# Optimization experiments

Hardware: AMD Instinct MI355X
Metric: run time of the kernel (lower is better)

The kernel has to match this reference:

```python
import jax, jax.numpy as jnp
import numpy as np

N_QUBITS = 16
DIM = 1 << N_QUBITS
NUM_CLASSES = 23
BATCH = 64

# PauliZ sign table: wire 0 is the most-significant bit of the flattened index.
_idx = np.arange(DIM)
SIGNS = np.stack([1 - 2 * ((_idx >> (N_QUBITS - 1 - w)) & 1) for w in range(N_QUBITS)], axis=1).astype(np.float32)  # (DIM, 16)


def _rx_mat(theta):
    c = jnp.cos(theta / 2).astype(jnp.complex64)
    s = (-1j * jnp.sin(theta / 2)).astype(jnp.complex64)
    return jnp.stack([jnp.stack([c, s]), jnp.stack([s, c])])  # (2,2)


def _rot_mat(phi, theta, omega):
    ct = jnp.cos(theta / 2)
    st = jnp.sin(theta / 2)
    a = jnp.exp(-0.5j * (phi + omega)) * ct
    b = -jnp.exp(0.5j * (phi - omega)) * st
    c = jnp.exp(-0.5j * (phi - omega)) * st
    d = jnp.exp(0.5j * (phi + omega)) * ct
    return jnp.stack([jnp.stack([a, b]), jnp.stack([c, d])]).astype(jnp.complex64)


def _apply_1q(state, U, w):
    # state: (B, 2,...,2); shared 2x2 gate on wire w (axis w+1)
    st = jnp.tensordot(state, U, axes=[[w + 1], [1]])  # contracted axis moves to last
    return jnp.moveaxis(st, -1, w + 1)


def _apply_rx_batched(state, theta_b, w):
    # per-sample RX angles theta_b: (B,)
    half = theta_b / 2
    c = jnp.cos(half).astype(jnp.complex64)
    s = (-1j * jnp.sin(half)).astype(jnp.complex64)
    U = jnp.stack([jnp.stack([c, s], -1), jnp.stack([s, c], -1)], -2)  # (B,2,2)
    st = jnp.moveaxis(state, w + 1, -1)
    st = jnp.einsum('bji,b...i->b...j', U, st)
    return jnp.moveaxis(st, -1, w + 1)


def _apply_crx(state, theta, ctrl, tgt):
    s0 = jax.lax.index_in_dim(state, 0, axis=ctrl + 1, keepdims=False)
    s1 = jax.lax.index_in_dim(state, 1, axis=ctrl + 1, keepdims=False)
    tax = tgt + 1 if tgt < ctrl else tgt  # target axis after control axis removal
    U = _rx_mat(theta)
    s1 = jnp.moveaxis(jnp.tensordot(s1, U, axes=[[tax], [1]]), -1, tax)
    return jnp.stack([s0, s1], axis=ctrl + 1)


def _circuit(x, w0, x0, w1, x1):
    B = x.shape[0]
    state = jnp.zeros((B,) + (2,) * N_QUBITS, jnp.complex64)
    state = state.at[(slice(None),) + (0,) * N_QUBITS].set(1.0)
    for w, xc in ((w0, x0), (w1, x1)):
        for q in range(N_QUBITS):
            state = _apply_rx_batched(state, x[:, q], q)
        for q in range(N_QUBITS):
            state = _apply_1q(state, _rot_mat(w[q, 0], w[q, 1], w[q, 2]), q)
        for q in range(N_QUBITS):
            state = _apply_crx(state, xc[q], q, (q + 1) % N_QUBITS)
    probs = (state.real ** 2 + state.imag ** 2).reshape(B, DIM)
    return probs @ jnp.asarray(SIGNS)  # (B, 16) PauliZ expvals


def setup_inputs() -> dict:
    key = jax.random.key(0)
    ks = jax.random.split(key, 7)
    return {
        'x': jax.random.normal(ks[0], (BATCH, N_QUBITS), jnp.float32),
        'w0': jax.random.normal(ks[1], (N_QUBITS, 3), jnp.float32),
        'x0': jax.random.normal(ks[2], (N_QUBITS,), jnp.float32),
        'w1': jax.random.normal(ks[3], (N_QUBITS, 3), jnp.float32),
        'x1': jax.random.normal(ks[4], (N_QUBITS,), jnp.float32),
        'fc_w': jax.random.normal(ks[5], (NUM_CLASSES, N_QUBITS), jnp.float32) * 0.25,
        'fc_b': jax.random.normal(ks[6], (NUM_CLASSES,), jnp.float32) * 0.05,
    }


def reference(x, w0, x0, w1, x1, fc_w, fc_b):
    feats = _circuit(x, w0, x0, w1, x1)           # (B, 16)
    logits = feats @ fc_w.T + fc_b                # (B, 23)
    return jax.nn.log_softmax(logits, axis=1)
```

## Files before the change

### kernel.cpp

```cpp
#include <hip/hip_runtime.h>
#include <hip/hip_bf16.h>


#define NQ 16
#define DIM 65536
#define BATCH 64
#define PSTR 544


template<int RB>
__device__ __forceinline__ void g1q_reg(float* sr, float* si, const float* U) {
  float u00r=U[0],u00i=U[1],u01r=U[2],u01i=U[3],u10r=U[4],u10i=U[5],u11r=U[6],u11i=U[7];
#pragma unroll
  for (int k = 0; k < 8; ++k) {
    int lo = k & ((1<<RB)-1);
    int j0 = ((k >> RB) << (RB+1)) | lo;
    int j1 = j0 | (1<<RB);
    float a0r=sr[j0], a0i=si[j0], a1r=sr[j1], a1i=si[j1];
    sr[j0] = u00r*a0r - u00i*a0i + u01r*a1r - u01i*a1i;
    si[j0] = u00r*a0i + u00i*a0r + u01r*a1i + u01i*a1r;
    sr[j1] = u10r*a0r - u10i*a0i + u11r*a1r - u11i*a1i;
    si[j1] = u10r*a0i + u10i*a0r + u11r*a1i + u11i*a1r;
  }
}

template<int RB, int CB>
__device__ __forceinline__ void gsel_reg_cc(float* sr, float* si, const float* M0, const float* M1) {
  float a0=M0[0],a1=M0[1],a2=M0[2],a3=M0[3],a4=M0[4],a5=M0[5],a6=M0[6],a7=M0[7];
  float b0=M1[0],b1=M1[1],b2=M1[2],b3=M1[3],b4=M1[4],b5=M1[5],b6=M1[6],b7=M1[7];
#pragma unroll
  for (int k = 0; k < 8; ++k) {
    int lo = k & ((1<<RB)-1);
    int j0 = ((k >> RB) << (RB+1)) | lo;
    int j1 = j0 | (1<<RB);
    const bool c = ((j0 >> CB) & 1) != 0;
    float u00r=c?b0:a0, u00i=c?b1:a1, u01r=c?b2:a2, u01i=c?b3:a3;
    float u10r=c?b4:a4, u10i=c?b5:a5, u11r=c?b6:a6, u11i=c?b7:a7;
    float p0r=sr[j0], p0i=si[j0], p1r=sr[j1], p1i=si[j1];
    sr[j0] = u00r*p0r - u00i*p0i + u01r*p1r - u01i*p1i;
    si[j0] = u00r*p0i + u00i*p0r + u01r*p1i + u01i*p1r;
    sr[j1] = u10r*p0r - u10i*p0i + u11r*p1r - u11i*p1i;
    si[j1] = u10r*p0i + u10i*p0r + u11r*p1i + u11i*p1r;
  }
}

template<int RB>
__device__ __forceinline__ void gsel_reg_pred(float* sr, float* si, const float* M0,
                                              const float* M1, bool ctrl) {
  float u[8];
#pragma unroll
  for (int e = 0; e < 8; ++e) u[e] = ctrl ? M1[e] : M0[e];
  g1q_reg<RB>(sr, si, u);
}

template<int LB, int CB>
__device__ __forceinline__ void gsel_lane_creg(float* sr, float* si, const float* M0,
                                               const float* M1, int lane) {
  int side = (lane >> LB) & 1;
  float d0r = side ? M0[6] : M0[0], d0i = side ? M0[7] : M0[1];
  float o0r = side ? M0[4] : M0[2], o0i = side ? M0[5] : M0[3];
  float d1r = side ? M1[6] : M1[0], d1i = side ? M1[7] : M1[1];
  float o1r = side ? M1[4] : M1[2], o1i = side ? M1[5] : M1[3];
#pragma unroll
  for (int j = 0; j < 16; ++j) {
    const bool c = ((j >> CB) & 1) != 0;
    float dr = c ? d1r : d0r, di = c ? d1i : d0i;
    float og = c ? o1r : o0r, oi = c ? o1i : o0i;
    float pr = __shfl_xor(sr[j], 1<<LB, 64);
    float pi = __shfl_xor(si[j], 1<<LB, 64);
    float mr = sr[j], mi = si[j];
    sr[j] = dr*mr - di*mi + og*pr - oi*pi;
    si[j] = dr*mi + di*mr + og*pi + oi*pr;
  }
}

template<int CB, int LB>
__device__ __forceinline__ void crx_reg_lane(float* sr, float* si, float c, float s) {
#pragma unroll
  for (int k = 0; k < 8; ++k) {
    int lo2 = k & ((1<<CB)-1);
    int j = ((((k >> CB) << (CB+1)) | lo2)) | (1<<CB);
    float pr = __shfl_xor(sr[j], 1<<LB, 64);
    float pi = __shfl_xor(si[j], 1<<LB, 64);
    float mr = sr[j], mi = si[j];
    sr[j] = c*mr + s*pi;
    si[j] = c*mi - s*pr;
  }
}

__device__ __forceinline__ int swz(int o) { return o ^ ((o>>4)&15) ^ ((o>>8)&15); }


__global__ void kprep(const float* __restrict__ x, const float* __restrict__ w0,
                      const float* __restrict__ x0, const float* __restrict__ w1,
                      const float* __restrict__ x1, float* __restrict__ P,
                      float* __restrict__ crxb, float* __restrict__ feats,
                      int* __restrict__ ctr) {
  __shared__ float su[32][8];
  int b = blockIdx.x;
  int t = threadIdx.x;
  if (t < 16) feats[b*16 + t] = 0.f;
  if (t == 16) ctr[b] = 0;
  if (t < 32) {
    int l = t >> 4, q = t & 15;
    const float* W = (l ? w1 : w0) + q*3;
    float xa = 0.5f * x[b*16 + q];
    float cr = cosf(xa), sx = sinf(xa);
    float phi = W[0], th = W[1], om = W[2];
    float ct = cosf(0.5f*th), stt = sinf(0.5f*th);
    float po = 0.5f*(phi+om), pm = 0.5f*(phi-om);
    float ar =  cosf(po)*ct,  ai = -sinf(po)*ct;
    float br = -cosf(pm)*stt, bi = -sinf(pm)*stt;
    float cr2 = cosf(pm)*stt, ci2 = -sinf(pm)*stt;
    float dr =  cosf(po)*ct,  di =  sinf(po)*ct;
    float U[8];
    U[0] = ar*cr + bi*sx;   U[1] = ai*cr - br*sx;
    U[2] = ai*sx + br*cr;   U[3] = -ar*sx + bi*cr;
    U[4] = cr2*cr + di*sx;  U[5] = ci2*cr - dr*sx;
    U[6] = ci2*sx + dr*cr;  U[7] = -cr2*sx + di*cr;
    float* M0 = P + (size_t)b*PSTR + ((l*16+q)*2+0)*8;
    float* M1 = M0 + 8;
#pragma unroll
    for (int e = 0; e < 8; ++e) { M0[e] = U[e]; su[t][e] = U[e]; }
    if (q == 0) {
      float ang = l ? 0.5f*x0[15] : 0.f;
      float cg = cosf(ang), sg = sinf(ang);
      M1[0] =  cg*U[0] + sg*U[3];  M1[1] = cg*U[1] - sg*U[2];
      M1[2] =  sg*U[1] + cg*U[2];  M1[3] = -sg*U[0] + cg*U[3];
      M1[4] =  cg*U[4] + sg*U[7];  M1[5] = cg*U[5] - sg*U[6];
      M1[6] =  sg*U[5] + cg*U[6];  M1[7] = -sg*U[4] + cg*U[7];
    } else {
      float ang = 0.5f*(l ? x1[q-1] : x0[q-1]);
      float cg = cosf(ang), sg = sinf(ang);
      M1[0] = cg*U[0] + sg*U[5];  M1[1] = cg*U[1] - sg*U[4];
      M1[2] = cg*U[2] + sg*U[7];  M1[3] = cg*U[3] - sg*U[6];
      M1[4] = cg*U[4] + sg*U[1];  M1[5] = cg*U[5] - sg*U[0];
      M1[6] = cg*U[6] + sg*U[3];  M1[7] = cg*U[7] - sg*U[2];
    }
    if (b == 0 && t == 0) { crxb[0] = cosf(0.5f*x1[15]); crxb[1] = sinf(0.5f*x1[15]); }
  }
  __syncthreads();
  if (t == 0) {
    float T0r[8], T0i[8], T1r[8], T1i[8];
#pragma unroll
    for (int k = 0; k < 8; ++k) {
      int b2 = (k>>2)&1, b1 = (k>>1)&1, b0k = k&1;
      float xr = su[13][b2*4], xi = su[13][b2*4+1];
      float yr = su[14][b1*4], yi = su[14][b1*4+1];
      float zr = su[15][b0k*4], zi = su[15][b0k*4+1];
      float pr = xr*yr - xi*yi, pi = xr*yi + xi*yr;
      T0r[k] = pr*zr - pi*zi; T0i[k] = pr*zi + pi*zr;
    }
    float a12 = 0.5f*x0[12], c12 = cosf(a12), s12 = sinf(a12);
#pragma unroll
    for (int k = 0; k < 8; ++k) { T1r[k] = c12*T0r[k] + s12*T0i[k^4]; T1i[k] = c12*T0i[k] - s12*T0r[k^4]; }
    float a13 = 0.5f*x0[13], c13 = cosf(a13), s13 = sinf(a13);
    float n0r[8], n0i[8], n1r[8], n1i[8];
#pragma unroll
    for (int k = 0; k < 8; ++k) {
      if (k & 4) {
        n0r[k] = c13*T0r[k] + s13*T0i[k^2]; n0i[k] = c13*T0i[k] - s13*T0r[k^2];
        n1r[k] = c13*T1r[k] + s13*T1i[k^2]; n1i[k] = c13*T1i[k] - s13*T1r[k^2];
      } else { n0r[k]=T0r[k]; n0i[k]=T0i[k]; n1r[k]=T1r[k]; n1i[k]=T1i[k]; }
    }
    float a14 = 0.5f*x0[14], c14 = cosf(a14), s14 = sinf(a14);
    float* T0 = P + (size_t)b*PSTR + 512;
    float* T1 = T0 + 16;
#pragma unroll
    for (int k = 0; k < 8; ++k) {
      float r0, i0, r1, i1;
      if (k & 2) {
        r0 = c14*n0r[k] + s14*n0i[k^1]; i0 = c14*n0i[k] - s14*n0r[k^1];
        r1 = c14*n1r[k] + s14*n1i[k^1]; i1 = c14*n1i[k] - s14*n1r[k^1];
      } else { r0=n0r[k]; i0=n0i[k]; r1=n1r[k]; i1=n1i[k]; }
      T0[2*k] = r0; T0[2*k+1] = i0; T1[2*k] = r1; T1[2*k+1] = i1;
    }
  }
}

#define MP(Pb, l, q, s) ((Pb) + (((l)*16+(q))*2+(s))*8)


__global__ __launch_bounds__(512) void pA(float4* __restrict__ cst4, const float* __restrict__ P) {
  __shared__ float2 lds2[8192];
  int b = blockIdx.x;
  int t = threadIdx.x, lane = t & 63, wv = t >> 6;
  const float* Pb = P + (size_t)b*PSTR;

  float sr[16], si[16];
#pragma unroll
  for (int r = 0; r < 16; ++r) { sr[r] = 0.f; si[r] = 0.f; }
  if (t == 0) sr[0] = 1.f;

  g1q_reg<3>(sr, si, MP(Pb,0,0,0));
  gsel_reg_cc<2,3>(sr, si, MP(Pb,0,1,0), MP(Pb,0,1,1));
  gsel_reg_cc<1,2>(sr, si, MP(Pb,0,2,0), MP(Pb,0,2,1));
  gsel_reg_cc<0,1>(sr, si, MP(Pb,0,3,0), MP(Pb,0,3,1));

#pragma unroll
  for (int r = 0; r < 16; ++r) {
    int o = wv | (lane << 3) | (r << 9);
    lds2[swz(o)] = make_float2(sr[r], si[r]);
  }
  __syncthreads();
#pragma unroll
  for (int r = 0; r < 16; ++r) {
    int o = wv | (((lane>>4)&3) << 3) | (r << 5) | ((lane&15) << 9);
    float2 v = lds2[swz(o)]; sr[r] = v.x; si[r] = v.y;
  }

  gsel_reg_pred<3>(sr, si, MP(Pb,0,4,0), MP(Pb,0,4,1), (lane&1)!=0);
  gsel_reg_cc<2,3>(sr, si, MP(Pb,0,5,0), MP(Pb,0,5,1));
  gsel_reg_cc<1,2>(sr, si, MP(Pb,0,6,0), MP(Pb,0,6,1));
  gsel_reg_cc<0,1>(sr, si, MP(Pb,0,7,0), MP(Pb,0,7,1));

  __syncthreads();
#pragma unroll
  for (int r = 0; r < 16; ++r) {
    int o = wv | (((lane>>4)&3) << 3) | (r << 5) | ((lane&15) << 9);
    lds2[swz(o)] = make_float2(sr[r], si[r]);
  }
  __syncthreads();
#pragma unroll
  for (int r = 0; r < 16; ++r) {
    int o = (lane&1) | (r << 1) | (((lane>>1)&31) << 5) | (wv << 10);
    float2 v = lds2[swz(o)]; sr[r] = v.x; si[r] = v.y;
  }

  gsel_reg_pred<3>(sr, si, MP(Pb,0,8,0), MP(Pb,0,8,1), (lane&2)!=0);
  gsel_reg_cc<2,3>(sr, si, MP(Pb,0,9,0), MP(Pb,0,9,1));
  gsel_reg_cc<1,2>(sr, si, MP(Pb,0,10,0), MP(Pb,0,10,1));
  gsel_reg_cc<0,1>(sr, si, MP(Pb,0,11,0), MP(Pb,0,11,1));
  gsel_lane_creg<0,0>(sr, si, MP(Pb,0,12,0), MP(Pb,0,12,1), lane);

  __syncthreads();
#pragma unroll
  for (int r = 0; r < 16; ++r) {
    int o = (lane&1) | (r << 1) | (((lane>>1)&31) << 5) | (wv << 10);
    lds2[swz(o)] = make_float2(sr[r], si[r]);
  }
  __syncthreads();
#pragma unroll
  for (int r = 0; r < 16; ++r) {
    int o = ((wv>>2)&1) | (lane << 1) | ((wv&3) << 7) | (r << 9);
    float2 v = lds2[swz(o)]; sr[r] = v.x; si[r] = v.y;
  }
  {
    int base4 = (lane << 3) | ((wv&3) << 9) | (((wv>>2)&1) << 11);
    float4* dst = cst4 + (size_t)b*4096 + base4;
#pragma unroll
    for (int g = 0; g < 8; ++g)
      dst[g] = make_float4(sr[2*g], si[2*g], sr[2*g+1], si[2*g+1]);
  }
}


__global__ __launch_bounds__(512) void pB(float2* __restrict__ st, const float4* __restrict__ cst4,
                                          const float* __restrict__ P) {
  __shared__ float2 lds2[8192];
  int blk = blockIdx.x;
  int b = blk >> 3, m = blk & 7;
  int t = threadIdx.x, lane = t & 63, wv = t >> 6;
  const float* Pb = P + (size_t)b*PSTR;

  float sr[16], si[16];
  {
    const float4* src = cst4 + (size_t)b*4096 + ((lane << 3) | ((wv&3) << 9) | (((m>>2)&1) << 11));
    const float* Ts = ((m>>2)&1) ? (Pb + 528) : (Pb + 512);
    int k = ((wv>>2)&1) | ((m&1) << 1) | (((m>>1)&1) << 2);
    float tr = Ts[2*k], ti = Ts[2*k+1];
#pragma unroll
    for (int g = 0; g < 8; ++g) {
      float4 v = src[g];
      sr[2*g]   = tr*v.x - ti*v.y;  si[2*g]   = tr*v.y + ti*v.x;
      sr[2*g+1] = tr*v.z - ti*v.w;  si[2*g+1] = tr*v.w + ti*v.z;
    }
  }

  gsel_reg_pred<3>(sr, si, MP(Pb,1,0,0), MP(Pb,1,0,1), ((wv>>2)&1)!=0);
  gsel_reg_cc<2,3>(sr, si, MP(Pb,1,1,0), MP(Pb,1,1,1));
  gsel_reg_cc<1,2>(sr, si, MP(Pb,1,2,0), MP(Pb,1,2,1));
  gsel_reg_cc<0,1>(sr, si, MP(Pb,1,3,0), MP(Pb,1,3,1));

#pragma unroll
  for (int r = 0; r < 16; ++r) {
    int o = (lane&63) | ((wv&3) << 6) | (r << 8) | (((wv>>2)&1) << 12);
    lds2[swz(o)] = make_float2(sr[r], si[r]);
  }
  __syncthreads();
#pragma unroll
  for (int r = 0; r < 16; ++r) {
    int o = (lane&15) | (r << 4) | (((lane>>4)&3) << 8) | ((wv&3) << 10) | (((wv>>2)&1) << 12);
    float2 v = lds2[swz(o)]; sr[r] = v.x; si[r] = v.y;
  }

  gsel_reg_pred<3>(sr, si, MP(Pb,1,4,0), MP(Pb,1,4,1), (lane&16)!=0);
  gsel_reg_cc<2,3>(sr, si, MP(Pb,1,5,0), MP(Pb,1,5,1));
  gsel_reg_cc<1,2>(sr, si, MP(Pb,1,6,0), MP(Pb,1,6,1));
  gsel_reg_cc<0,1>(sr, si, MP(Pb,1,7,0), MP(Pb,1,7,1));

  __syncthreads();
#pragma unroll
  for (int r = 0; r < 16; ++r) {
    int o = (lane&15) | (r << 4) | (((lane>>4)&3) << 8) | ((wv&3) << 10) | (((wv>>2)&1) << 12);
    lds2[swz(o)] = make_float2(sr[r], si[r]);
  }
  __syncthreads();
#pragma unroll
  for (int r = 0; r < 16; ++r) {
    int o = r | ((lane&63) << 4) | ((wv&3) << 10) | (((wv>>2)&1) << 12);
    float2 v = lds2[swz(o)]; sr[r] = v.x; si[r] = v.y;
  }

  gsel_reg_pred<3>(sr, si, MP(Pb,1,8,0), MP(Pb,1,8,1), (lane&1)!=0);
  gsel_reg_cc<2,3>(sr, si, MP(Pb,1,9,0), MP(Pb,1,9,1));
  gsel_reg_cc<1,2>(sr, si, MP(Pb,1,10,0), MP(Pb,1,10,1));
  gsel_reg_cc<0,1>(sr, si, MP(Pb,1,11,0), MP(Pb,1,11,1));

  {
    int sbase = ((lane&63) << 4) | ((wv&3) << 10) | (((wv>>2)&1) << 12) | (m << 13);
    float4* dst = (float4*)(st + (size_t)b*DIM + sbase);
#pragma unroll
    for (int g = 0; g < 8; ++g)
      dst[g] = make_float4(sr[2*g], si[2*g], sr[2*g+1], si[2*g+1]);
  }
}


__global__ __launch_bounds__(512) void p3(const float2* __restrict__ st, const float* __restrict__ P,
                                          const float* __restrict__ crxb, float* __restrict__ feats,
                                          int* __restrict__ ctr, const float* __restrict__ fcw,
                                          const float* __restrict__ fcb, float* __restrict__ out) {
  int blk = blockIdx.x;
  int b = blk >> 3, n = blk & 7;
  int t = threadIdx.x, lane = t & 63, wv = t >> 6;
  const float* Pb = P + (size_t)b*PSTR;
  int base = (lane&31) | (wv << 5) | (n << 8) | ((lane>>5) << 11);
  const float2* S = st + (size_t)b*DIM + base;
  float sr[16], si[16];
#pragma unroll
  for (int r = 0; r < 16; ++r) { float2 v = S[r << 12]; sr[r] = v.x; si[r] = v.y; }

  gsel_reg_pred<3>(sr, si, MP(Pb,1,12,0), MP(Pb,1,12,1), (lane&1)!=0);
  gsel_reg_cc<2,3>(sr, si, MP(Pb,1,13,0), MP(Pb,1,13,1));
  gsel_reg_cc<1,2>(sr, si, MP(Pb,1,14,0), MP(Pb,1,14,1));
  gsel_reg_cc<0,1>(sr, si, MP(Pb,1,15,0), MP(Pb,1,15,1));
  crx_reg_lane<0,5>(sr, si, crxb[0], crxb[1]);

  float tot=0.f, sA=0.f, sB=0.f, sC=0.f, sD=0.f;
#pragma unroll
  for (int r = 0; r < 16; ++r) {
    float p = sr[r]*sr[r] + si[r]*si[r];
    tot += p;
    sA += (r & 1) ? -p : p;
    sB += (r & 2) ? -p : p;
    sC += (r & 4) ? -p : p;
    sD += (r & 8) ? -p : p;
  }
  float f[16];
  f[15] = sA; f[14] = sB; f[13] = sC; f[12] = sD;
  f[11] = (lane&1)  ? -tot : tot;
  f[10] = (lane&2)  ? -tot : tot;
  f[9]  = (lane&4)  ? -tot : tot;
  f[8]  = (lane&8)  ? -tot : tot;
  f[7]  = (lane&16) ? -tot : tot;
  f[0]  = (lane&32) ? -tot : tot;
  f[6]  = (wv&1)    ? -tot : tot;
  f[5]  = (wv&2)    ? -tot : tot;
  f[4]  = (wv&4)    ? -tot : tot;
  f[3]  = (n&1)     ? -tot : tot;
  f[2]  = (n&2)     ? -tot : tot;
  f[1]  = (n&4)     ? -tot : tot;
#pragma unroll
  for (int w = 0; w < 16; ++w) {
#pragma unroll
    for (int off = 32; off; off >>= 1) f[w] += __shfl_xor(f[w], off, 64);
  }
  __shared__ float red[8][17];
  if (lane == 0) {
#pragma unroll
    for (int w = 0; w < 16; ++w) red[wv][w] = f[w];
  }
  __syncthreads();
  if (t < 16) {
    float acc = 0.f;
#pragma unroll
    for (int i = 0; i < 8; ++i) acc += red[i][t];
    atomicAdd(&feats[b*16 + t], acc);
  }

  __shared__ int flagS;
  __syncthreads();
  if (t == 0) { __threadfence(); flagS = atomicAdd(&ctr[b], 1); }
  __syncthreads();
  if (flagS == 7) {
    __shared__ float fs[16];
    __shared__ float lg[23];
    if (t < 16) fs[t] = __hip_atomic_load(&feats[b*16 + t], __ATOMIC_RELAXED, __HIP_MEMORY_SCOPE_AGENT);
    __syncthreads();
    if (t < 23) {
      float acc = fcb[t];
#pragma unroll
      for (int w = 0; w < 16; ++w) acc += fs[w] * fcw[t*16 + w];
      lg[t] = acc;
    }
    __syncthreads();
    if (t < 23) {
      float mx = -1e30f;
#pragma unroll
      for (int j = 0; j < 23; ++j) mx = fmaxf(mx, lg[j]);
      float Ssum = 0.f;
#pragma unroll
      for (int j = 0; j < 23; ++j) Ssum += expf(lg[j] - mx);
      out[b*23 + t] = lg[t] - mx - logf(Ssum);
    }
  }
}

extern "C" void kernel_launch(void* const* d_in, const int* in_sizes, int n_in,
                              void* d_out, int out_size, void* d_ws, size_t ws_size,
                              hipStream_t stream) {
  const float* x   = (const float*)d_in[0];
  const float* w0  = (const float*)d_in[1];
  const float* x0  = (const float*)d_in[2];
  const float* w1  = (const float*)d_in[3];
  const float* x1  = (const float*)d_in[4];
  const float* fcw = (const float*)d_in[5];
  const float* fcb = (const float*)d_in[6];
  float* out = (float*)d_out;

  char* ws = (char*)d_ws;
  float2* st   = (float2*)ws;
  float4* cst4 = (float4*)(ws + (size_t)BATCH * DIM * sizeof(float2));
  float*  P    = (float*)((char*)cst4 + (size_t)BATCH * 8192 * sizeof(float2));
  float*  crxb = P + (size_t)BATCH * PSTR;
  float*  feats = crxb + 16;
  int*    ctr  = (int*)(feats + BATCH*16);

  kprep<<<BATCH, 64, 0, stream>>>(x, w0, x0, w1, x1, P, crxb, feats, ctr);
  pA<<<BATCH, 512, 0, stream>>>(cst4, P);
  pB<<<512, 512, 0, stream>>>(st, cst4, P);
  p3<<<512, 512, 0, stream>>>(st, P, crxb, feats, ctr, fcw, fcb, out);
  (void)in_sizes; (void)n_in; (void)out_size; (void)ws_size;
}
```

Measured before the change: 140.1 us.

## Fuse gate prep into pA and store intermediate state as packed bf16

Moves the per-sample gate-matrix preparation kernel into the start of pA, removing one launch. The prepared matrices go to global memory and each block reads them back after a barrier, with the CRX constants now stored in the per-sample parameter block. The intermediate state vector between pB and p3 is now written as packed bf16 real/imag pairs instead of float2, halving that global traffic. In exchange, the final layers' amplitudes lose precision, which could push the expectation values outside tolerance.

```diff
diff --git a/kernel.cpp b/kernel.cpp
--- a/kernel.cpp
+++ b/kernel.cpp
@@ -2,10 +2,9 @@
 #include <hip/hip_bf16.h>
 
 
-#define NQ 16
 #define DIM 65536
 #define BATCH 64
-#define PSTR 544
+#define PSTR 548
 
 
 template<int RB>
@@ -90,102 +89,108 @@
 
 __device__ __forceinline__ int swz(int o) { return o ^ ((o>>4)&15) ^ ((o>>8)&15); }
 
-
-__global__ void kprep(const float* __restrict__ x, const float* __restrict__ w0,
-                      const float* __restrict__ x0, const float* __restrict__ w1,
-                      const float* __restrict__ x1, float* __restrict__ P,
-                      float* __restrict__ crxb, float* __restrict__ feats,
-                      int* __restrict__ ctr) {
-  __shared__ float su[32][8];
-  int b = blockIdx.x;
-  int t = threadIdx.x;
-  if (t < 16) feats[b*16 + t] = 0.f;
-  if (t == 16) ctr[b] = 0;
-  if (t < 32) {
-    int l = t >> 4, q = t & 15;
-    const float* W = (l ? w1 : w0) + q*3;
-    float xa = 0.5f * x[b*16 + q];
-    float cr = cosf(xa), sx = sinf(xa);
-    float phi = W[0], th = W[1], om = W[2];
-    float ct = cosf(0.5f*th), stt = sinf(0.5f*th);
-    float po = 0.5f*(phi+om), pm = 0.5f*(phi-om);
-    float ar =  cosf(po)*ct,  ai = -sinf(po)*ct;
-    float br = -cosf(pm)*stt, bi = -sinf(pm)*stt;
-    float cr2 = cosf(pm)*stt, ci2 = -sinf(pm)*stt;
-    float dr =  cosf(po)*ct,  di =  sinf(po)*ct;
-    float U[8];
-    U[0] = ar*cr + bi*sx;   U[1] = ai*cr - br*sx;
-    U[2] = ai*sx + br*cr;   U[3] = -ar*sx + bi*cr;
-    U[4] = cr2*cr + di*sx;  U[5] = ci2*cr - dr*sx;
-    U[6] = ci2*sx + dr*cr;  U[7] = -cr2*sx + di*cr;
-    float* M0 = P + (size_t)b*PSTR + ((l*16+q)*2+0)*8;
-    float* M1 = M0 + 8;
-#pragma unroll
-    for (int e = 0; e < 8; ++e) { M0[e] = U[e]; su[t][e] = U[e]; }
-    if (q == 0) {
-      float ang = l ? 0.5f*x0[15] : 0.f;
-      float cg = cosf(ang), sg = sinf(ang);
-      M1[0] =  cg*U[0] + sg*U[3];  M1[1] = cg*U[1] - sg*U[2];
-      M1[2] =  sg*U[1] + cg*U[2];  M1[3] = -sg*U[0] + cg*U[3];
-      M1[4] =  cg*U[4] + sg*U[7];  M1[5] = cg*U[5] - sg*U[6];
-      M1[6] =  sg*U[5] + cg*U[6];  M1[7] = -sg*U[4] + cg*U[7];
-    } else {
-      float ang = 0.5f*(l ? x1[q-1] : x0[q-1]);
-      float cg = cosf(ang), sg = sinf(ang);
-      M1[0] = cg*U[0] + sg*U[5];  M1[1] = cg*U[1] - sg*U[4];
-      M1[2] = cg*U[2] + sg*U[7];  M1[3] = cg*U[3] - sg*U[6];
-      M1[4] = cg*U[4] + sg*U[1];  M1[5] = cg*U[5] - sg*U[0];
-      M1[6] = cg*U[6] + sg*U[3];  M1[7] = cg*U[7] - sg*U[2];
-    }
-    if (b == 0 && t == 0) { crxb[0] = cosf(0.5f*x1[15]); crxb[1] = sinf(0.5f*x1[15]); }
-  }
-  __syncthreads();
-  if (t == 0) {
-    float T0r[8], T0i[8], T1r[8], T1i[8];
-#pragma unroll
-    for (int k = 0; k < 8; ++k) {
-      int b2 = (k>>2)&1, b1 = (k>>1)&1, b0k = k&1;
-      float xr = su[13][b2*4], xi = su[13][b2*4+1];
-      float yr = su[14][b1*4], yi = su[14][b1*4+1];
-      float zr = su[15][b0k*4], zi = su[15][b0k*4+1];
-      float pr = xr*yr - xi*yi, pi = xr*yi + xi*yr;
-      T0r[k] = pr*zr - pi*zi; T0i[k] = pr*zi + pi*zr;
-    }
-    float a12 = 0.5f*x0[12], c12 = cosf(a12), s12 = sinf(a12);
-#pragma unroll
-    for (int k = 0; k < 8; ++k) { T1r[k] = c12*T0r[k] + s12*T0i[k^4]; T1i[k] = c12*T0i[k] - s12*T0r[k^4]; }
-    float a13 = 0.5f*x0[13], c13 = cosf(a13), s13 = sinf(a13);
-    float n0r[8], n0i[8], n1r[8], n1i[8];
-#pragma unroll
-    for (int k = 0; k < 8; ++k) {
-      if (k & 4) {
-        n0r[k] = c13*T0r[k] + s13*T0i[k^2]; n0i[k] = c13*T0i[k] - s13*T0r[k^2];
-        n1r[k] = c13*T1r[k] + s13*T1i[k^2]; n1i[k] = c13*T1i[k] - s13*T1r[k^2];
-      } else { n0r[k]=T0r[k]; n0i[k]=T0i[k]; n1r[k]=T1r[k]; n1i[k]=T1i[k]; }
-    }
-    float a14 = 0.5f*x0[14], c14 = cosf(a14), s14 = sinf(a14);
-    float* T0 = P + (size_t)b*PSTR + 512;
-    float* T1 = T0 + 16;
-#pragma unroll
-    for (int k = 0; k < 8; ++k) {
-      float r0, i0, r1, i1;
-      if (k & 2) {
-        r0 = c14*n0r[k] + s14*n0i[k^1]; i0 = c14*n0i[k] - s14*n0r[k^1];
-        r1 = c14*n1r[k] + s14*n1i[k^1]; i1 = c14*n1i[k] - s14*n1r[k^1];
-      } else { r0=n0r[k]; i0=n0i[k]; r1=n1r[k]; i1=n1i[k]; }
-      T0[2*k] = r0; T0[2*k+1] = i0; T1[2*k] = r1; T1[2*k+1] = i1;
-    }
-  }
-}
+__device__ __forceinline__ unsigned bfp(float r, float i) {
+  unsigned ur = __float_as_uint(r), ui = __float_as_uint(i);
+  ur = (ur + 0x7fffu + ((ur >> 16) & 1u)) >> 16;
+  ui = (ui + 0x7fffu + ((ui >> 16) & 1u)) & 0xffff0000u;
+  return (ur & 0xffffu) | ui;
+}
+__device__ __forceinline__ float bfr(unsigned u) { return __uint_as_float(u << 16); }
+__device__ __forceinline__ float bfi(unsigned u) { return __uint_as_float(u & 0xffff0000u); }
 
 #define MP(Pb, l, q, s) ((Pb) + (((l)*16+(q))*2+(s))*8)
 
 
-__global__ __launch_bounds__(512) void pA(float4* __restrict__ cst4, const float* __restrict__ P) {
+__global__ __launch_bounds__(512) void pA(float4* __restrict__ cst4, float* __restrict__ P,
+                                          const float* __restrict__ x, const float* __restrict__ w0,
+                                          const float* __restrict__ x0, const float* __restrict__ w1,
+                                          const float* __restrict__ x1, float* __restrict__ feats,
+                                          int* __restrict__ ctr) {
   __shared__ float2 lds2[8192];
   int b = blockIdx.x;
   int t = threadIdx.x, lane = t & 63, wv = t >> 6;
-  const float* Pb = P + (size_t)b*PSTR;
+  float* Pb = P + (size_t)b * PSTR;
+
+  {
+    float (*su)[8] = reinterpret_cast<float(*)[8]>(lds2);
+    if (t < 16) feats[b*16 + t] = 0.f;
+    if (t == 16) ctr[b] = 0;
+    if (t < 32) {
+      int l = t >> 4, q = t & 15;
+      const float* W = (l ? w1 : w0) + q*3;
+      float xa = 0.5f * x[b*16 + q];
+      float cr = cosf(xa), sx = sinf(xa);
+      float phi = W[0], th = W[1], om = W[2];
+      float ct = cosf(0.5f*th), stt = sinf(0.5f*th);
+      float po = 0.5f*(phi+om), pm = 0.5f*(phi-om);
+      float ar =  cosf(po)*ct,  ai = -sinf(po)*ct;
+      float br = -cosf(pm)*stt, bi = -sinf(pm)*stt;
+      float cr2 = cosf(pm)*stt, ci2 = -sinf(pm)*stt;
+      float dr =  cosf(po)*ct,  di =  sinf(po)*ct;
+      float U[8];
+      U[0] = ar*cr + bi*sx;   U[1] = ai*cr - br*sx;
+      U[2] = ai*sx + br*cr;   U[3] = -ar*sx + bi*cr;
+      U[4] = cr2*cr + di*sx;  U[5] = ci2*cr - dr*sx;
+      U[6] = ci2*sx + dr*cr;  U[7] = -cr2*sx + di*cr;
+      float* M0 = MP(Pb, l, q, 0);
+      float* M1 = M0 + 8;
+#pragma unroll
+      for (int e = 0; e < 8; ++e) { M0[e] = U[e]; su[t][e] = U[e]; }
+      if (q == 0) {
+        float ang = l ? 0.5f*x0[15] : 0.f;
+        float cg = cosf(ang), sg = sinf(ang);
+        M1[0] =  cg*U[0] + sg*U[3];  M1[1] = cg*U[1] - sg*U[2];
+        M1[2] =  sg*U[1] + cg*U[2];  M1[3] = -sg*U[0] + cg*U[3];
+        M1[4] =  cg*U[4] + sg*U[7];  M1[5] = cg*U[5] - sg*U[6];
+        M1[6] =  sg*U[5] + cg*U[6];  M1[7] = -sg*U[4] + cg*U[7];
+      } else {
+        float ang = 0.5f*(l ? x1[q-1] : x0[q-1]);
+        float cg = cosf(ang), sg = sinf(ang);
+        M1[0] = cg*U[0] + sg*U[5];  M1[1] = cg*U[1] - sg*U[4];
+        M1[2] = cg*U[2] + sg*U[7];  M1[3] = cg*U[3] - sg*U[6];
+        M1[4] = cg*U[4] + sg*U[1];  M1[5] = cg*U[5] - sg*U[0];
+        M1[6] = cg*U[6] + sg*U[3];  M1[7] = cg*U[7] - sg*U[2];
+      }
+      if (t == 0) { Pb[546] = cosf(0.5f*x1[15]); Pb[547] = sinf(0.5f*x1[15]); }
+    }
+    __syncthreads();
+    if (t == 0) {
+      float T0r[8], T0i[8], T1r[8], T1i[8];
+#pragma unroll
+      for (int k = 0; k < 8; ++k) {
+        int b2 = (k>>2)&1, b1 = (k>>1)&1, b0k = k&1;
+        float xr = su[13][b2*4], xi = su[13][b2*4+1];
+        float yr = su[14][b1*4], yi = su[14][b1*4+1];
+        float zr = su[15][b0k*4], zi = su[15][b0k*4+1];
+        float pr = xr*yr - xi*yi, pi = xr*yi + xi*yr;
+        T0r[k] = pr*zr - pi*zi; T0i[k] = pr*zi + pi*zr;
+      }
+      float a12 = 0.5f*x0[12], c12 = cosf(a12), s12 = sinf(a12);
+#pragma unroll
+      for (int k = 0; k < 8; ++k) { T1r[k] = c12*T0r[k] + s12*T0i[k^4]; T1i[k] = c12*T0i[k] - s12*T0r[k^4]; }
+      float a13 = 0.5f*x0[13], c13 = cosf(a13), s13 = sinf(a13);
+      float n0r[8], n0i[8], n1r[8], n1i[8];
+#pragma unroll
+      for (int k = 0; k < 8; ++k) {
+        if (k & 4) {
+          n0r[k] = c13*T0r[k] + s13*T0i[k^2]; n0i[k] = c13*T0i[k] - s13*T0r[k^2];
+          n1r[k] = c13*T1r[k] + s13*T1i[k^2]; n1i[k] = c13*T1i[k] - s13*T1r[k^2];
+        } else { n0r[k]=T0r[k]; n0i[k]=T0i[k]; n1r[k]=T1r[k]; n1i[k]=T1i[k]; }
+      }
+      float a14 = 0.5f*x0[14], c14 = cosf(a14), s14 = sinf(a14);
+      float* T0 = Pb + 512;
+      float* T1 = Pb + 528;
+#pragma unroll
+      for (int k = 0; k < 8; ++k) {
+        float r0, i0, r1, i1;
+        if (k & 2) {
+          r0 = c14*n0r[k] + s14*n0i[k^1]; i0 = c14*n0i[k] - s14*n0r[k^1];
+          r1 = c14*n1r[k] + s14*n1i[k^1]; i1 = c14*n1i[k] - s14*n1r[k^1];
+        } else { r0=n0r[k]; i0=n0i[k]; r1=n1r[k]; i1=n1i[k]; }
+        T0[2*k] = r0; T0[2*k+1] = i0; T1[2*k] = r1; T1[2*k+1] = i1;
+      }
+    }
+  }
 
   float sr[16], si[16];
 #pragma unroll
@@ -196,7 +201,7 @@
   gsel_reg_cc<2,3>(sr, si, MP(Pb,0,1,0), MP(Pb,0,1,1));
   gsel_reg_cc<1,2>(sr, si, MP(Pb,0,2,0), MP(Pb,0,2,1));
   gsel_reg_cc<0,1>(sr, si, MP(Pb,0,3,0), MP(Pb,0,3,1));
-
+  __syncthreads();
 #pragma unroll
   for (int r = 0; r < 16; ++r) {
     int o = wv | (lane << 3) | (r << 9);
@@ -208,12 +213,10 @@
     int o = wv | (((lane>>4)&3) << 3) | (r << 5) | ((lane&15) << 9);
     float2 v = lds2[swz(o)]; sr[r] = v.x; si[r] = v.y;
   }
-
   gsel_reg_pred<3>(sr, si, MP(Pb,0,4,0), MP(Pb,0,4,1), (lane&1)!=0);
   gsel_reg_cc<2,3>(sr, si, MP(Pb,0,5,0), MP(Pb,0,5,1));
   gsel_reg_cc<1,2>(sr, si, MP(Pb,0,6,0), MP(Pb,0,6,1));
   gsel_reg_cc<0,1>(sr, si, MP(Pb,0,7,0), MP(Pb,0,7,1));
-
   __syncthreads();
 #pragma unroll
   for (int r = 0; r < 16; ++r) {
@@ -226,13 +229,11 @@
     int o = (lane&1) | (r << 1) | (((lane>>1)&31) << 5) | (wv << 10);
     float2 v = lds2[swz(o)]; sr[r] = v.x; si[r] = v.y;
   }
-
   gsel_reg_pred<3>(sr, si, MP(Pb,0,8,0), MP(Pb,0,8,1), (lane&2)!=0);
   gsel_reg_cc<2,3>(sr, si, MP(Pb,0,9,0), MP(Pb,0,9,1));
   gsel_reg_cc<1,2>(sr, si, MP(Pb,0,10,0), MP(Pb,0,10,1));
   gsel_reg_cc<0,1>(sr, si, MP(Pb,0,11,0), MP(Pb,0,11,1));
   gsel_lane_creg<0,0>(sr, si, MP(Pb,0,12,0), MP(Pb,0,12,1), lane);
-
   __syncthreads();
 #pragma unroll
   for (int r = 0; r < 16; ++r) {
@@ -255,7 +256,7 @@
 }
 
 
-__global__ __launch_bounds__(512) void pB(float2* __restrict__ st, const float4* __restrict__ cst4,
+__global__ __launch_bounds__(512) void pB(unsigned* __restrict__ st, const float4* __restrict__ cst4,
                                           const float* __restrict__ P) {
   __shared__ float2 lds2[8192];
   int blk = blockIdx.x;
@@ -276,12 +277,10 @@
       sr[2*g+1] = tr*v.z - ti*v.w;  si[2*g+1] = tr*v.w + ti*v.z;
     }
   }
-
   gsel_reg_pred<3>(sr, si, MP(Pb,1,0,0), MP(Pb,1,0,1), ((wv>>2)&1)!=0);
   gsel_reg_cc<2,3>(sr, si, MP(Pb,1,1,0), MP(Pb,1,1,1));
   gsel_reg_cc<1,2>(sr, si, MP(Pb,1,2,0), MP(Pb,1,2,1));
   gsel_reg_cc<0,1>(sr, si, MP(Pb,1,3,0), MP(Pb,1,3,1));
-
 #pragma unroll
   for (int r = 0; r < 16; ++r) {
     int o = (lane&63) | ((wv&3) << 6) | (r << 8) | (((wv>>2)&1) << 12);
@@ -293,12 +292,10 @@
     int o = (lane&15) | (r << 4) | (((lane>>4)&3) << 8) | ((wv&3) << 10) | (((wv>>2)&1) << 12);
     float2 v = lds2[swz(o)]; sr[r] = v.x; si[r] = v.y;
   }
-
   gsel_reg_pred<3>(sr, si, MP(Pb,1,4,0), MP(Pb,1,4,1), (lane&16)!=0);
   gsel_reg_cc<2,3>(sr, si, MP(Pb,1,5,0), MP(Pb,1,5,1));
   gsel_reg_cc<1,2>(sr, si, MP(Pb,1,6,0), MP(Pb,1,6,1));
   gsel_reg_cc<0,1>(sr, si, MP(Pb,1,7,0), MP(Pb,1,7,1));
-
   __syncthreads();
 #pragma unroll
   for (int r = 0; r < 16; ++r) {
@@ -311,41 +308,40 @@
     int o = r | ((lane&63) << 4) | ((wv&3) << 10) | (((wv>>2)&1) << 12);
     float2 v = lds2[swz(o)]; sr[r] = v.x; si[r] = v.y;
   }
-
   gsel_reg_pred<3>(sr, si, MP(Pb,1,8,0), MP(Pb,1,8,1), (lane&1)!=0);
   gsel_reg_cc<2,3>(sr, si, MP(Pb,1,9,0), MP(Pb,1,9,1));
   gsel_reg_cc<1,2>(sr, si, MP(Pb,1,10,0), MP(Pb,1,10,1));
   gsel_reg_cc<0,1>(sr, si, MP(Pb,1,11,0), MP(Pb,1,11,1));
-
   {
     int sbase = ((lane&63) << 4) | ((wv&3) << 10) | (((wv>>2)&1) << 12) | (m << 13);
-    float4* dst = (float4*)(st + (size_t)b*DIM + sbase);
-#pragma unroll
-    for (int g = 0; g < 8; ++g)
-      dst[g] = make_float4(sr[2*g], si[2*g], sr[2*g+1], si[2*g+1]);
-  }
-}
-
-
-__global__ __launch_bounds__(512) void p3(const float2* __restrict__ st, const float* __restrict__ P,
-                                          const float* __restrict__ crxb, float* __restrict__ feats,
-                                          int* __restrict__ ctr, const float* __restrict__ fcw,
-                                          const float* __restrict__ fcb, float* __restrict__ out) {
+    uint4* dst = (uint4*)(st + (size_t)b*DIM + sbase);
+#pragma unroll
+    for (int g = 0; g < 4; ++g)
+      dst[g] = make_uint4(bfp(sr[4*g],si[4*g]), bfp(sr[4*g+1],si[4*g+1]),
+                          bfp(sr[4*g+2],si[4*g+2]), bfp(sr[4*g+3],si[4*g+3]));
+  }
+}
+
+
+__global__ __launch_bounds__(512) void p3(const unsigned* __restrict__ st, const float* __restrict__ P,
+                                          float* __restrict__ feats, int* __restrict__ ctr,
+                                          const float* __restrict__ fcw, const float* __restrict__ fcb,
+                                          float* __restrict__ out) {
   int blk = blockIdx.x;
   int b = blk >> 3, n = blk & 7;
   int t = threadIdx.x, lane = t & 63, wv = t >> 6;
   const float* Pb = P + (size_t)b*PSTR;
   int base = (lane&31) | (wv << 5) | (n << 8) | ((lane>>5) << 11);
-  const float2* S = st + (size_t)b*DIM + base;
+  const unsigned* S = st + (size_t)b*DIM + base;
   float sr[16], si[16];
 #pragma unroll
-  for (int r = 0; r < 16; ++r) { float2 v = S[r << 12]; sr[r] = v.x; si[r] = v.y; }
+  for (int r = 0; r < 16; ++r) { unsigned u = S[r << 12]; sr[r] = bfr(u); si[r] = bfi(u); }
 
   gsel_reg_pred<3>(sr, si, MP(Pb,1,12,0), MP(Pb,1,12,1), (lane&1)!=0);
   gsel_reg_cc<2,3>(sr, si, MP(Pb,1,13,0), MP(Pb,1,13,1));
   gsel_reg_cc<1,2>(sr, si, MP(Pb,1,14,0), MP(Pb,1,14,1));
   gsel_reg_cc<0,1>(sr, si, MP(Pb,1,15,0), MP(Pb,1,15,1));
-  crx_reg_lane<0,5>(sr, si, crxb[0], crxb[1]);
+  crx_reg_lane<0,5>(sr, si, Pb[546], Pb[547]);
 
   float tot=0.f, sA=0.f, sB=0.f, sC=0.f, sD=0.f;
 #pragma unroll
@@ -430,16 +426,14 @@
   float* out = (float*)d_out;
 
   char* ws = (char*)d_ws;
-  float2* st   = (float2*)ws;
-  float4* cst4 = (float4*)(ws + (size_t)BATCH * DIM * sizeof(float2));
-  float*  P    = (float*)((char*)cst4 + (size_t)BATCH * 8192 * sizeof(float2));
-  float*  crxb = P + (size_t)BATCH * PSTR;
-  float*  feats = crxb + 16;
-  int*    ctr  = (int*)(feats + BATCH*16);
-
-  kprep<<<BATCH, 64, 0, stream>>>(x, w0, x0, w1, x1, P, crxb, feats, ctr);
-  pA<<<BATCH, 512, 0, stream>>>(cst4, P);
+  unsigned* st  = (unsigned*)ws;
+  float4* cst4  = (float4*)(ws + (size_t)BATCH * DIM * 4);
+  float*  P     = (float*)((char*)cst4 + (size_t)BATCH * 8192 * 8);
+  float*  feats = P + (size_t)BATCH * PSTR;
+  int*    ctr   = (int*)(feats + BATCH*16);
+
+  pA<<<BATCH, 512, 0, stream>>>(cst4, P, x, w0, x0, w1, x1, feats, ctr);
   pB<<<512, 512, 0, stream>>>(st, cst4, P);
-  p3<<<512, 512, 0, stream>>>(st, P, crxb, feats, ctr, fcw, fcb, out);
+  p3<<<512, 512, 0, stream>>>(st, P, feats, ctr, fcw, fcb, out);
   (void)in_sizes; (void)n_in; (void)out_size; (void)ws_size;
 }
```

After: 130.5 us. 1.07x faster.
